# Kernel tuning notes

Measured on AMD Instinct MI355X. Metric: run time of the kernel, lower is better.

Reference implementation:

```python
import jax, jax.numpy as jnp
import numpy as np

N = 50000
E = 800000
F_IN = 128
HEADS = 4
C_OUT = 32
NEG_SLOPE = 0.2


def setup_inputs() -> dict:
    key = jax.random.key(0)
    k_x, k_e, k_w, k_as, k_ad, k_b = jax.random.split(key, 6)
    x = jax.random.normal(k_x, (N, F_IN), dtype=jnp.float32)
    edge_index = jax.random.randint(k_e, (2, E), 0, N, dtype=jnp.int32)
    # Glorot-style init for linear weight [F_IN, HEADS*C_OUT] and attention vectors.
    scale_w = 1.0 / np.sqrt(F_IN)
    W = jax.random.normal(k_w, (F_IN, HEADS * C_OUT), dtype=jnp.float32) * scale_w
    scale_a = 1.0 / np.sqrt(C_OUT)
    att_src = jax.random.normal(k_as, (HEADS, C_OUT), dtype=jnp.float32) * scale_a
    att_dst = jax.random.normal(k_ad, (HEADS, C_OUT), dtype=jnp.float32) * scale_a
    bias = jnp.zeros((HEADS * C_OUT,), dtype=jnp.float32)
    return {"x": x, "edge_index": edge_index, "W": W, "att_src": att_src,
            "att_dst": att_dst, "bias": bias}


def reference(x, edge_index, W, att_src, att_dst, bias):
    n = x.shape[0]
    # add self loops (PyG add_self_loops=True)
    loops = jnp.arange(n, dtype=edge_index.dtype)
    src = jnp.concatenate([edge_index[0], loops])  # [E+N]
    dst = jnp.concatenate([edge_index[1], loops])  # [E+N]
    edge_index_full = jnp.stack([src, dst])

    h = (x @ W).reshape(n, HEADS, C_OUT)           # [N,H,C]
    a_src = jnp.einsum('nhc,hc->nh', h, att_src)   # [N,H]
    a_dst = jnp.einsum('nhc,hc->nh', h, att_dst)   # [N,H]

    e = jax.nn.leaky_relu(a_src[src] + a_dst[dst], NEG_SLOPE)  # [E',H]
    # segment softmax over edges grouped by destination node
    m = jax.ops.segment_max(e, dst, num_segments=n)            # [N,H]
    e = jnp.exp(e - m[dst])
    s = jax.ops.segment_sum(e, dst, num_segments=n)            # [N,H]
    alpha = e / (s[dst] + 1e-16)                               # [E',H]

    msg = h[src] * alpha[:, :, None]                           # [E',H,C]
    out = jax.ops.segment_sum(msg, dst, num_segments=n)        # [N,H,C]
    out = out.reshape(n, HEADS * C_OUT) + bias                 # concat=True
    return out, edge_index_full, alpha
```

## Files before the change

### kernel.cpp

```cpp
#include <hip/hip_runtime.h>

#define NNODES 50000
#define NEDGES 800000
#define ETOT   (NEDGES + NNODES)
#define FIN    128
#define FOUT   128
#define HEADS  4
#define NEG    0.2f
#define RCAP   64
#define WSTR   136
#define NBUCK  196
#define CAPB   4608

typedef float  f32x4 __attribute__((ext_vector_type(4)));
typedef int    i32x4 __attribute__((ext_vector_type(4)));
typedef short  s16x8 __attribute__((ext_vector_type(8)));
typedef unsigned short u16x8 __attribute__((ext_vector_type(8)));

__device__ __forceinline__ float lrelu(float v) { return v > 0.f ? v : NEG * v; }
__device__ __forceinline__ float4 e4(float4 a, float4 b) {
    return make_float4(__expf(lrelu(a.x + b.x)), __expf(lrelu(a.y + b.y)),
                       __expf(lrelu(a.z + b.z)), __expf(lrelu(a.w + b.w)));
}
__device__ __forceinline__ unsigned short f2bf(float f) {
    unsigned u = __float_as_uint(f);
    return (unsigned short)((u + 0x7FFFu + ((u >> 16) & 1u)) >> 16);
}
__device__ __forceinline__ void nt_store4(float* p, float a, float b, float c, float d) {
    f32x4 v = {a, b, c, d};
    __builtin_nontemporal_store(v, (f32x4*)p);
}

__global__ __launch_bounds__(256) void k_wt(const float* __restrict__ W,
                                            unsigned short* __restrict__ Wt,
                                            int* __restrict__ gcnt)
{
    if (blockIdx.x == 0 && threadIdx.x < NBUCK) gcnt[threadIdx.x] = 0;
    const int i = blockIdx.x * 256 + threadIdx.x;
    const int c = i & 127, kq = i >> 7;
    const int k0 = kq * 4;
    ushort4 v;
    v.x = f2bf(W[(k0 + 0) * 128 + c]);
    v.y = f2bf(W[(k0 + 1) * 128 + c]);
    v.z = f2bf(W[(k0 + 2) * 128 + c]);
    v.w = f2bf(W[(k0 + 3) * 128 + c]);
    *(ushort4*)(Wt + c * 128 + k0) = v;
}

__global__ __launch_bounds__(256) void k_gemm(
    const float* __restrict__ x, const unsigned short* __restrict__ Wtg,
    const float* __restrict__ att_s, const float* __restrict__ att_d,
    unsigned short* __restrict__ hb, float* __restrict__ a_src, float* __restrict__ a_dst)
{
    __shared__ unsigned short Wl[128 * WSTR];
    __shared__ unsigned short Xl[64 * WSTR];

    const int tid = threadIdx.x;
    const int nbase = blockIdx.x * 64;

    for (int i = tid; i < 2048; i += 256) {
        int c = i >> 4, q = i & 15;
        *(u16x8*)(&Wl[c * WSTR + q * 8]) = *(const u16x8*)(&Wtg[c * 128 + q * 8]);
    }
#pragma unroll
    for (int it = 0; it < 8; it++) {
        int flat = it * 256 + tid;
        int row = flat >> 5, kq = flat & 31;
        int gn = nbase + row; if (gn >= NNODES) gn = NNODES - 1;
        float4 v = *(const float4*)(x + (size_t)gn * FIN + kq * 4);
        ushort4 b;
        b.x = f2bf(v.x); b.y = f2bf(v.y); b.z = f2bf(v.z); b.w = f2bf(v.w);
        *(ushort4*)(&Xl[row * WSTR + kq * 4]) = b;
    }
    __syncthreads();

    const int wid = tid >> 6, lane = tid & 63;
    const int r16 = lane & 15;
    const int kg  = lane >> 4;

    s16x8 af[4];
#pragma unroll
    for (int t = 0; t < 4; t++)
        af[t] = *(const s16x8*)(&Xl[(wid * 16 + r16) * WSTR + t * 32 + kg * 8]);

    float pa[4] = {0.f, 0.f, 0.f, 0.f};
    float pd[4] = {0.f, 0.f, 0.f, 0.f};

#pragma unroll
    for (int cg = 0; cg < 8; cg++) {
        s16x8 bf[4];
#pragma unroll
        for (int t = 0; t < 4; t++)
            bf[t] = *(const s16x8*)(&Wl[(cg * 16 + r16) * WSTR + t * 32 + kg * 8]);
        f32x4 acc = {0.f, 0.f, 0.f, 0.f};
#pragma unroll
        for (int t = 0; t < 4; t++)
            acc = __builtin_amdgcn_mfma_f32_16x16x32_bf16(af[t], bf[t], acc, 0, 0, 0);

        const int col = cg * 16 + r16;
        const float asv = att_s[col], adv = att_d[col];
#pragma unroll
        for (int i2 = 0; i2 < 4; i2++) {
            int node = nbase + wid * 16 + kg * 4 + i2;
            if (node < NNODES)
                hb[(size_t)node * FOUT + col] = f2bf(acc[i2]);
            pa[i2] = fmaf(acc[i2], asv, pa[i2]);
            pd[i2] = fmaf(acc[i2], adv, pd[i2]);
        }
        if (cg & 1) {
            const int head = cg >> 1;
#pragma unroll
            for (int i2 = 0; i2 < 4; i2++) {
                float a = pa[i2], d = pd[i2];
                a += __shfl_xor(a, 1); a += __shfl_xor(a, 2);
                a += __shfl_xor(a, 4); a += __shfl_xor(a, 8);
                d += __shfl_xor(d, 1); d += __shfl_xor(d, 2);
                d += __shfl_xor(d, 4); d += __shfl_xor(d, 8);
                if (r16 == 0) {
                    int node = nbase + wid * 16 + kg * 4 + i2;
                    if (node < NNODES) {
                        a_src[node * HEADS + head] = a;
                        a_dst[node * HEADS + head] = d;
                    }
                }
                pa[i2] = 0.f; pd[i2] = 0.f;
            }
        }
    }
}

__global__ __launch_bounds__(256) void k_bin(
    const int* __restrict__ ei, int* __restrict__ gcnt, unsigned* __restrict__ region)
{
    __shared__ int lcnt[NBUCK], lpos[NBUCK], gbase[NBUCK];
    const int tid = threadIdx.x;
    const int q0 = blockIdx.x * 1024;

    if (tid < NBUCK) lcnt[tid] = 0;
    __syncthreads();

    i32x4 sq[4], dq[4];
    bool v[4];
#pragma unroll
    for (int j = 0; j < 4; j++) {
        const int q = q0 + tid + j * 256;
        v[j] = (q < NEDGES / 4);
        const int qi = v[j] ? q : 0;
        sq[j] = ((const i32x4*)ei)[qi];
        dq[j] = ((const i32x4*)(ei + NEDGES))[qi];
    }
#pragma unroll
    for (int j = 0; j < 4; j++)
        if (v[j]) {
#pragma unroll
            for (int c = 0; c < 4; c++) atomicAdd(&lcnt[dq[j][c] >> 8], 1);
        }
    __syncthreads();
    if (tid < NBUCK) { gbase[tid] = atomicAdd(&gcnt[tid], lcnt[tid]); lpos[tid] = 0; }
    __syncthreads();
#pragma unroll
    for (int j = 0; j < 4; j++)
        if (v[j]) {
#pragma unroll
            for (int c = 0; c < 4; c++) {
                const int d = dq[j][c], b = d >> 8;
                const int idx = gbase[b] + atomicAdd(&lpos[b], 1);
                if (idx < CAPB)
                    region[(size_t)b * CAPB + idx] =
                        (unsigned)sq[j][c] | ((unsigned)(d & 255) << 16);
            }
        }
}

__global__ __launch_bounds__(256) void k_asm(
    const unsigned* __restrict__ region, const int* __restrict__ gcnt,
    int* __restrict__ cnt, unsigned short* __restrict__ csr16)
{
    __shared__ unsigned short rows[256 * RCAP];
    __shared__ int lcnt[256];
    const int tid = threadIdx.x;
    const int b = blockIdx.x;
    lcnt[tid] = 0;
    __syncthreads();

    const int m = min(gcnt[b], CAPB);
    for (int i = tid; i < m; i += 256) {
        const unsigned u = region[(size_t)b * CAPB + i];
        const int dl = u >> 16;
        const int sl = atomicAdd(&lcnt[dl], 1);
        if (sl < RCAP) rows[dl * RCAP + sl] = (unsigned short)(u & 0xFFFFu);
    }
    __syncthreads();

    const int nodebase = b * 256;
    const int nrows = min(256, NNODES - nodebase);
    for (int i = tid; i < nrows * 8; i += 256) {
        const int r = i >> 3, q = i & 7;
        *(u16x8*)(&csr16[((size_t)(nodebase + r) << 6) + q * 8]) =
            *(const u16x8*)(&rows[r * RCAP + q * 8]);
    }
    if (tid < nrows) cnt[nodebase + tid] = lcnt[tid];
}

__global__ __launch_bounds__(256) void k_msg(
    const unsigned short* __restrict__ hb, const float* __restrict__ a_src,
    const float* __restrict__ a_dst, const int* __restrict__ cnt,
    const unsigned short* __restrict__ csr16, const float* __restrict__ bias,
    float* __restrict__ out, float* __restrict__ nd)
{
    const int tid = threadIdx.x;
    const int wid = tid >> 6, lane = tid & 63;
    const int n = blockIdx.x * 4 + wid;
    __shared__ unsigned short slds[4][RCAP];
    __shared__ float elds[4][RCAP * 4];

    const int deg_r = min(cnt[n], RCAP - 1);
    const int deg = deg_r + 1;
    const float4 ad = ((const float4*)a_dst)[n];

    unsigned s = (unsigned)n;
    float4 ev = make_float4(0.f, 0.f, 0.f, 0.f);
    if (lane < deg) {
        if (lane < deg_r) s = csr16[(n << 6) + lane];
        float4 as = ((const float4*)a_src)[s];
        ev = e4(as, ad);
    }
    float4 den = ev;
#pragma unroll
    for (int o = 32; o >= 1; o >>= 1) {
        den.x += __shfl_xor(den.x, o);
        den.y += __shfl_xor(den.y, o);
        den.z += __shfl_xor(den.z, o);
        den.w += __shfl_xor(den.w, o);
    }
    const float4 inv = make_float4(1.f / (den.x + 1e-16f), 1.f / (den.y + 1e-16f),
                                   1.f / (den.z + 1e-16f), 1.f / (den.w + 1e-16f));
    if (lane == 0) {
        ((float4*)nd)[n * 2]     = ad;
        ((float4*)nd)[n * 2 + 1] = inv;
    }
    slds[wid][lane] = (unsigned short)s;
    ((float4*)elds[wid])[lane] =
        make_float4(ev.x * inv.x, ev.y * inv.y, ev.z * inv.z, ev.w * inv.w);

    const int sub = lane >> 4;
    const int c8  = lane & 15;
    const int head = c8 >> 2;
    const char* hbase = (const char*)hb;
    float acc[8];
#pragma unroll
    for (int j = 0; j < 8; j++) acc[j] = 0.f;
    const int dp = (deg + 3) & ~3;
    for (int base = 0; base < dp; base += 4) {
        const int i = base + sub;
        const float al = elds[wid][i * 4 + head];
        const unsigned si = slds[wid][i];
        const float4 u = *(const float4*)(hbase + si * 256u + c8 * 16u);
        const unsigned u0 = __float_as_uint(u.x), u1 = __float_as_uint(u.y);
        const unsigned u2 = __float_as_uint(u.z), u3 = __float_as_uint(u.w);
        acc[0] = fmaf(__uint_as_float(u0 << 16),          al, acc[0]);
        acc[1] = fmaf(__uint_as_float(u0 & 0xFFFF0000u),  al, acc[1]);
        acc[2] = fmaf(__uint_as_float(u1 << 16),          al, acc[2]);
        acc[3] = fmaf(__uint_as_float(u1 & 0xFFFF0000u),  al, acc[3]);
        acc[4] = fmaf(__uint_as_float(u2 << 16),          al, acc[4]);
        acc[5] = fmaf(__uint_as_float(u2 & 0xFFFF0000u),  al, acc[5]);
        acc[6] = fmaf(__uint_as_float(u3 << 16),          al, acc[6]);
        acc[7] = fmaf(__uint_as_float(u3 & 0xFFFF0000u),  al, acc[7]);
    }
#pragma unroll
    for (int j = 0; j < 8; j++) {
        acc[j] += __shfl_xor(acc[j], 16);
        acc[j] += __shfl_xor(acc[j], 32);
    }
    if (lane < 16) {
        const float4 b0 = ((const float4*)bias)[c8 * 2];
        const float4 b1 = ((const float4*)bias)[c8 * 2 + 1];
        ((float4*)out)[(size_t)n * 32 + c8 * 2] =
            make_float4(acc[0] + b0.x, acc[1] + b0.y, acc[2] + b0.z, acc[3] + b0.w);
        ((float4*)out)[(size_t)n * 32 + c8 * 2 + 1] =
            make_float4(acc[4] + b1.x, acc[5] + b1.y, acc[6] + b1.z, acc[7] + b1.w);
    }
}

__global__ __launch_bounds__(256) void k_alpha(
    const int* __restrict__ ei, const float* __restrict__ a_src,
    const float* __restrict__ nd, float* __restrict__ alpha,
    float* __restrict__ out_edge)
{
    const int i4 = blockIdx.x * blockDim.x + threadIdx.x;
    if (i4 >= ETOT / 4) return;
    i32x4 s4, d4;
    if (i4 < NEDGES / 4) {
        s4 = __builtin_nontemporal_load(&((const i32x4*)ei)[i4]);
        d4 = __builtin_nontemporal_load(&((const i32x4*)ei)[NEDGES / 4 + i4]);
    } else {
        const int n0 = i4 * 4 - NEDGES;
        s4 = d4 = (i32x4){n0, n0 + 1, n0 + 2, n0 + 3};
    }
    nt_store4(out_edge + (size_t)i4 * 4,
              (float)s4.x, (float)s4.y, (float)s4.z, (float)s4.w);
    nt_store4(out_edge + (size_t)(ETOT / 4 + i4) * 4,
              (float)d4.x, (float)d4.y, (float)d4.z, (float)d4.w);

    const float4* as4p = (const float4*)a_src;
    const float4* nd4p = (const float4*)nd;
#pragma unroll
    for (int j = 0; j < 4; j++) {
        const int s = s4[j];
        const int d = d4[j];
        float4 as = as4p[s];
        float4 ad = nd4p[d * 2];
        float4 iv = nd4p[d * 2 + 1];
        float4 ev = e4(as, ad);
        nt_store4(alpha + ((size_t)i4 * 4 + j) * 4,
                  ev.x * iv.x, ev.y * iv.y, ev.z * iv.z, ev.w * iv.w);
    }
}

extern "C" void kernel_launch(void* const* d_in, const int* in_sizes, int n_in,
                              void* d_out, int out_size, void* d_ws, size_t ws_size,
                              hipStream_t stream)
{
    const float* x     = (const float*)d_in[0];
    const int*   ei    = (const int*)  d_in[1];
    const float* W     = (const float*)d_in[2];
    const float* att_s = (const float*)d_in[3];
    const float* att_d = (const float*)d_in[4];
    const float* bias  = (const float*)d_in[5];

    unsigned short* hb = (unsigned short*)d_ws;
    float* a_src  = (float*)(hb + (size_t)NNODES * FOUT);
    float* a_dst  = a_src + NNODES * HEADS;
    float* nd     = a_dst + NNODES * HEADS;
    int*   cnt    = (int*)(nd + (size_t)NNODES * 8);
    unsigned short* csr16 = (unsigned short*)(cnt + NNODES);
    unsigned short* wt    = csr16 + (size_t)NNODES * RCAP;
    int*      gcnt  = (int*)(wt + 16384);
    unsigned* region = (unsigned*)(gcnt + 256);

    float* out_x = (float*)d_out;
    float* out_e = out_x + (size_t)NNODES * FOUT;
    float* out_a = out_e + (size_t)2 * ETOT;

    k_wt   <<<16, 256, 0, stream>>>(W, wt, gcnt);
    k_gemm <<<(NNODES + 63) / 64, 256, 0, stream>>>(x, wt, att_s, att_d, hb, a_src, a_dst);
    k_bin  <<<(NEDGES / 4 + 1023) / 1024, 256, 0, stream>>>(ei, gcnt, region);
    k_asm  <<<NBUCK, 256, 0, stream>>>(region, gcnt, cnt, csr16);
    k_msg  <<<NNODES / 4, 256, 0, stream>>>(hb, a_src, a_dst, cnt, csr16, bias, out_x, nd);
    k_alpha<<<(ETOT / 4 + 255) / 256, 256, 0, stream>>>(ei, a_src, nd, out_a, out_e);
}
```

Before: 105.9 us.

## Stage binned edges in LDS for coalesced scatter; software-pipeline message gather

The binning kernel now sorts each block's edge records by bucket in shared memory, using a block-wide prefix scan. It then writes them to the global bucket regions in contiguous runs instead of scattering each record individually, which should improve write coalescing. Records now carry the full destination index, so the assembly kernel masks out the local row. Separately, the message aggregation loop prefetches the next neighbor's feature row before doing the FMAs on the current one, to hide gather latency. The costs are an extra scan with many barriers, extra LDS use, and a few more registers in the message kernel.

```diff
diff --git a/kernel.cpp b/kernel.cpp
--- a/kernel.cpp
+++ b/kernel.cpp
@@ -132,11 +132,12 @@
 __global__ __launch_bounds__(256) void k_bin(
     const int* __restrict__ ei, int* __restrict__ gcnt, unsigned* __restrict__ region)
 {
-    __shared__ int lcnt[NBUCK], lpos[NBUCK], gbase[NBUCK];
+    __shared__ int lcnt[256], lofs[256], gbase[256], lpos[256], scan[256];
+    __shared__ unsigned recs[4096];
     const int tid = threadIdx.x;
     const int q0 = blockIdx.x * 1024;
 
-    if (tid < NBUCK) lcnt[tid] = 0;
+    lcnt[tid] = 0;
     __syncthreads();
 
     i32x4 sq[4], dq[4];
@@ -156,7 +157,17 @@
             for (int c = 0; c < 4; c++) atomicAdd(&lcnt[dq[j][c] >> 8], 1);
         }
     __syncthreads();
-    if (tid < NBUCK) { gbase[tid] = atomicAdd(&gcnt[tid], lcnt[tid]); lpos[tid] = 0; }
+    scan[tid] = lcnt[tid];
+    __syncthreads();
+    for (int o = 1; o < 256; o <<= 1) {
+        int t = (tid >= o) ? scan[tid - o] : 0;
+        __syncthreads();
+        scan[tid] += t;
+        __syncthreads();
+    }
+    lofs[tid] = scan[tid] - lcnt[tid];
+    if (tid < NBUCK) gbase[tid] = atomicAdd(&gcnt[tid], lcnt[tid]);
+    lpos[tid] = 0;
     __syncthreads();
 #pragma unroll
     for (int j = 0; j < 4; j++)
@@ -164,12 +175,18 @@
 #pragma unroll
             for (int c = 0; c < 4; c++) {
                 const int d = dq[j][c], b = d >> 8;
-                const int idx = gbase[b] + atomicAdd(&lpos[b], 1);
-                if (idx < CAPB)
-                    region[(size_t)b * CAPB + idx] =
-                        (unsigned)sq[j][c] | ((unsigned)(d & 255) << 16);
+                const int idx = lofs[b] + atomicAdd(&lpos[b], 1);
+                recs[idx] = (unsigned)sq[j][c] | ((unsigned)d << 16);
             }
         }
+    __syncthreads();
+    const int m = scan[255];
+    for (int i = tid; i < m; i += 256) {
+        const unsigned rec = recs[i];
+        const int b = rec >> 24;
+        const int off = gbase[b] + (i - lofs[b]);
+        if (off < CAPB) region[(size_t)b * CAPB + off] = rec;
+    }
 }
 
 __global__ __launch_bounds__(256) void k_asm(
@@ -186,7 +203,7 @@
     const int m = min(gcnt[b], CAPB);
     for (int i = tid; i < m; i += 256) {
         const unsigned u = region[(size_t)b * CAPB + i];
-        const int dl = u >> 16;
+        const int dl = (u >> 16) & 255;
         const int sl = atomicAdd(&lcnt[dl], 1);
         if (sl < RCAP) rows[dl * RCAP + sl] = (unsigned short)(u & 0xFFFFu);
     }
@@ -251,21 +268,42 @@
 #pragma unroll
     for (int j = 0; j < 8; j++) acc[j] = 0.f;
     const int dp = (deg + 3) & ~3;
-    for (int base = 0; base < dp; base += 4) {
-        const int i = base + sub;
-        const float al = elds[wid][i * 4 + head];
-        const unsigned si = slds[wid][i];
-        const float4 u = *(const float4*)(hbase + si * 256u + c8 * 16u);
-        const unsigned u0 = __float_as_uint(u.x), u1 = __float_as_uint(u.y);
-        const unsigned u2 = __float_as_uint(u.z), u3 = __float_as_uint(u.w);
-        acc[0] = fmaf(__uint_as_float(u0 << 16),          al, acc[0]);
-        acc[1] = fmaf(__uint_as_float(u0 & 0xFFFF0000u),  al, acc[1]);
-        acc[2] = fmaf(__uint_as_float(u1 << 16),          al, acc[2]);
-        acc[3] = fmaf(__uint_as_float(u1 & 0xFFFF0000u),  al, acc[3]);
-        acc[4] = fmaf(__uint_as_float(u2 << 16),          al, acc[4]);
-        acc[5] = fmaf(__uint_as_float(u2 & 0xFFFF0000u),  al, acc[5]);
-        acc[6] = fmaf(__uint_as_float(u3 << 16),          al, acc[6]);
-        acc[7] = fmaf(__uint_as_float(u3 & 0xFFFF0000u),  al, acc[7]);
+
+    int i0 = sub;
+    float al = elds[wid][i0 * 4 + head];
+    unsigned si = slds[wid][i0];
+    float4 u = *(const float4*)(hbase + si * 256u + c8 * 16u);
+
+    for (int base = 4; base < dp; base += 4) {
+        const int i1 = base + sub;
+        const float al2 = elds[wid][i1 * 4 + head];
+        const unsigned si2 = slds[wid][i1];
+        const float4 u2 = *(const float4*)(hbase + si2 * 256u + c8 * 16u);
+
+        const unsigned w0 = __float_as_uint(u.x), w1 = __float_as_uint(u.y);
+        const unsigned w2 = __float_as_uint(u.z), w3 = __float_as_uint(u.w);
+        acc[0] = fmaf(__uint_as_float(w0 << 16),          al, acc[0]);
+        acc[1] = fmaf(__uint_as_float(w0 & 0xFFFF0000u),  al, acc[1]);
+        acc[2] = fmaf(__uint_as_float(w1 << 16),          al, acc[2]);
+        acc[3] = fmaf(__uint_as_float(w1 & 0xFFFF0000u),  al, acc[3]);
+        acc[4] = fmaf(__uint_as_float(w2 << 16),          al, acc[4]);
+        acc[5] = fmaf(__uint_as_float(w2 & 0xFFFF0000u),  al, acc[5]);
+        acc[6] = fmaf(__uint_as_float(w3 << 16),          al, acc[6]);
+        acc[7] = fmaf(__uint_as_float(w3 & 0xFFFF0000u),  al, acc[7]);
+
+        u = u2; al = al2;
+    }
+    {
+        const unsigned w0 = __float_as_uint(u.x), w1 = __float_as_uint(u.y);
+        const unsigned w2 = __float_as_uint(u.z), w3 = __float_as_uint(u.w);
+        acc[0] = fmaf(__uint_as_float(w0 << 16),          al, acc[0]);
+        acc[1] = fmaf(__uint_as_float(w0 & 0xFFFF0000u),  al, acc[1]);
+        acc[2] = fmaf(__uint_as_float(w1 << 16),          al, acc[2]);
+        acc[3] = fmaf(__uint_as_float(w1 & 0xFFFF0000u),  al, acc[3]);
+        acc[4] = fmaf(__uint_as_float(w2 << 16),          al, acc[4]);
+        acc[5] = fmaf(__uint_as_float(w2 & 0xFFFF0000u),  al, acc[5]);
+        acc[6] = fmaf(__uint_as_float(w3 << 16),          al, acc[6]);
+        acc[7] = fmaf(__uint_as_float(w3 & 0xFFFF0000u),  al, acc[7]);
     }
 #pragma unroll
     for (int j = 0; j < 8; j++) {
```

Measured after the change: 104.1 us. Within noise of the previous version (-1.7%).
